# Performance work log

Hardware: AMD Instinct MI355X
Metric: run time of the kernel (lower is better)

The kernel has to match this reference:

```python
import jax, jax.numpy as jnp
import numpy as np

T, H, F, E, K = 4096, 2048, 1408, 8, 2  # tokens, hidden, intermediate, experts, top_k


def setup_inputs() -> dict:
    key = jax.random.key(0)
    k1, k2, k3, k4 = jax.random.split(key, 4)
    return {
        "hidden_states": jax.random.normal(k1, (T, H), dtype=jnp.float32),
        "router_logits": jax.random.normal(k2, (T, E), dtype=jnp.float32),
        # w1: (E, 2, H, F) where dim 1 = [gate_proj, up_proj]
        "w1": jax.random.normal(k3, (E, 2, H, F), dtype=jnp.float32) * 0.02,
        # w2: (E, F, H) down projection
        "w2": jax.random.normal(k4, (E, F, H), dtype=jnp.float32) * 0.02,
        "top_k": K,
    }


def reference(hidden_states, router_logits, w1, w2, top_k):
    # Router: softmax over all experts, then select top_k.
    # renormalize_topk_logits=False -> combine weights are the raw softmax probs.
    probs = jax.nn.softmax(router_logits, axis=-1)            # (T, E)
    topk_w, topk_ids = jax.lax.top_k(probs, top_k)            # (T, K) each

    num_experts = w1.shape[0]
    out = jnp.zeros_like(hidden_states)                       # (T, H)
    # Fixed small loop over experts (structurally distinct weight slices);
    # each expert's FFN is a dense GEMM over all tokens, masked by the
    # per-token combine coefficient (0 for tokens not routed to this expert).
    for e in range(num_experts):
        coef = jnp.sum(jnp.where(topk_ids == e, topk_w, 0.0), axis=-1)  # (T,)
        gate = hidden_states @ w1[e, 0]                       # (T, F)
        up = hidden_states @ w1[e, 1]                         # (T, F)
        h = jax.nn.silu(gate) * up                            # SwiGLU
        out = out + coef[:, None] * (h @ w2[e])               # (T, H)
    return out
```

## Files before the change

### kernel.cpp

```cpp
#include <hip/hip_runtime.h>
#include <stdint.h>

#define T_TOK 4096
#define HID   2048
#define FF    1408
#define NE    8
#define BUF   16384
#define NT1   (HID / 32)
#define NT2   (FF / 32)

typedef __attribute__((ext_vector_type(8))) short short8;
typedef __attribute__((ext_vector_type(4))) float f32x4;

__device__ inline unsigned short f2bf(float f) {
  uint32_t u = __builtin_bit_cast(uint32_t, f);
  u += 0x7fffu + ((u >> 16) & 1u);
  return (unsigned short)(u >> 16);
}

__device__ inline uint32_t cvt_pk(float a, float b) {
  uint32_t r;
  asm("v_cvt_pk_bf16_f32 %0, %1, %2" : "=v"(r) : "v"(a), "v"(b));
  return r;
}

__device__ inline void gload16(const void* g, void* l) {
  __builtin_amdgcn_global_load_lds(
      (const __attribute__((address_space(1))) unsigned int*)g,
      (__attribute__((address_space(3))) unsigned int*)l, 16, 0, 0);
}

__device__ inline void wait4_barrier() {
  asm volatile("s_waitcnt vmcnt(4)" ::: "memory");
  __builtin_amdgcn_s_barrier();
  asm volatile("" ::: "memory");
}
__device__ inline void wait0_barrier() {
  asm volatile("s_waitcnt vmcnt(0)" ::: "memory");
  __builtin_amdgcn_s_barrier();
  asm volatile("" ::: "memory");
}

__global__ __launch_bounds__(256) void route_kernel(const float* __restrict__ logits,
                                                    int2* __restrict__ eids,
                                                    float2* __restrict__ ecfs) {
  int t = blockIdx.x * 256 + threadIdx.x;
  const float4* lp = (const float4*)(logits + (size_t)t * NE);
  float4 a = lp[0], b = lp[1];
  float l[8] = {a.x, a.y, a.z, a.w, b.x, b.y, b.z, b.w};
  float mx = l[0];
#pragma unroll
  for (int i = 1; i < 8; ++i) mx = fmaxf(mx, l[i]);
  float s = 0.f, p[8];
#pragma unroll
  for (int i = 0; i < 8; ++i) { p[i] = __expf(l[i] - mx); s += p[i]; }
  float inv = 1.f / s;
  int e0 = 0;
#pragma unroll
  for (int i = 1; i < 8; ++i) if (l[i] > l[e0]) e0 = i;
  int e1 = (e0 == 0) ? 1 : 0;
#pragma unroll
  for (int i = 0; i < 8; ++i) if (i != e0 && l[i] > l[e1]) e1 = i;
  eids[t] = make_int2(e0, e1);
  ecfs[t] = make_float2(p[e0] * inv, p[e1] * inv);
}

__global__ __launch_bounds__(256) void compact_kernel(const int2* __restrict__ eids,
                                                      const float2* __restrict__ ecfs,
                                                      int* __restrict__ tok,
                                                      float* __restrict__ coef,
                                                      int* __restrict__ rowptr) {
  int e = blockIdx.x, tid = threadIdx.x;
  __shared__ int hist[8];
  __shared__ int wsum[4];
  __shared__ int runv;
  if (tid < 8) hist[tid] = 0;
  __syncthreads();
  for (int t = tid; t < T_TOK; t += 256) {
    int2 ei = eids[t];
    atomicAdd(&hist[ei.x], 1);
    atomicAdd(&hist[ei.y], 1);
  }
  __syncthreads();
  int off = 0;
  for (int j = 0; j < e; ++j) off += hist[j];
  if (tid == 0) {
    runv = 0;
    if (e == 0) rowptr[0] = 0;
    rowptr[e + 1] = off + hist[e];
  }
  __syncthreads();
  int wave = tid >> 6, lane = tid & 63;
  for (int c = 0; c < T_TOK; c += 256) {
    int t = c + tid;
    int2 ei = eids[t];
    float2 cf = ecfs[t];
    bool fl = false; float cv = 0.f;
    if (ei.x == e)      { fl = true; cv = cf.x; }
    else if (ei.y == e) { fl = true; cv = cf.y; }
    unsigned long long m = __ballot(fl);
    if (lane == 0) wsum[wave] = __popcll(m);
    __syncthreads();
    int woff = runv;
    for (int wv = 0; wv < wave; ++wv) woff += wsum[wv];
    int pos = off + woff + __popcll(m & ((1ull << lane) - 1ull));
    if (fl) { tok[pos] = t; coef[pos] = cv; }
    __syncthreads();
    if (tid == 0) runv += wsum[0] + wsum[1] + wsum[2] + wsum[3];
    __syncthreads();
  }
}

__global__ __launch_bounds__(256) void cvtx_kernel(const float* __restrict__ x,
                                                   unsigned short* __restrict__ xb) {
  int i = blockIdx.x * 256 + threadIdx.x;
  float4 v = ((const float4*)x)[i];
  uint2 o;
  o.x = cvt_pk(v.x, v.y);
  o.y = cvt_pk(v.z, v.w);
  ((uint2*)xb)[i] = o;
}

__global__ __launch_bounds__(256) void wcvt_kernel(const float* __restrict__ in,
                                                   unsigned short* __restrict__ out,
                                                   int R, int C) {
  __shared__ unsigned short t[64][72];
  const float* ip = in + ((size_t)blockIdx.z * R + blockIdx.y * 64) * C + blockIdx.x * 64;
  int tid = threadIdx.x;
  int r = tid >> 2, cg = (tid & 3) * 16;
  const float* rp = ip + (size_t)r * C + cg;
#pragma unroll
  for (int j = 0; j < 4; ++j) {
    float4 v = *(const float4*)(rp + j * 4);
    int c = cg + j * 4;
    t[c + 0][r] = f2bf(v.x);
    t[c + 1][r] = f2bf(v.y);
    t[c + 2][r] = f2bf(v.z);
    t[c + 3][r] = f2bf(v.w);
  }
  __syncthreads();
  int cr = tid >> 2, kg = (tid & 3) * 16;
  unsigned short* op = out + ((size_t)blockIdx.z * C + blockIdx.x * 64 + cr) * R +
                       blockIdx.y * 64 + kg;
  *(short8*)op = *(const short8*)&t[cr][kg];
  *(short8*)(op + 8) = *(const short8*)&t[cr][kg + 8];
}

__global__ __launch_bounds__(256) void gemm1_kernel(const unsigned short* __restrict__ Xb,
                                                    const unsigned short* __restrict__ w1t,
                                                    const int* __restrict__ tok,
                                                    const int* __restrict__ rowptr,
                                                    unsigned short* __restrict__ hbuf) {
  int f = blockIdx.x + 22 * blockIdx.y;
  int g = (f & 7) * 88 + (f >> 3);
  int ftile = g >> 5, mtile = g & 31;
  int e = blockIdx.z;
  int base = rowptr[e], cnt = rowptr[e + 1] - base;
  if (mtile * 128 >= cnt) return;
  __shared__ char smem[3 * BUF];
  int tid = threadIdx.x, lane = tid & 63, wave = tid >> 6;

  int rA = wave * 32 + (lane >> 2);
  int cd = (lane & 3) ^ ((rA >> 1) & 3);
  int sA0 = min(mtile * 128 + rA, cnt - 1);
  int sA1 = min(mtile * 128 + rA + 16, cnt - 1);
  const unsigned short* gA0 = Xb + (size_t)tok[base + sA0] * HID + cd * 8;
  const unsigned short* gA1 = Xb + (size_t)tok[base + sA1] * HID + cd * 8;
  int r1 = rA + 16;
  int p0 = (rA >> 4) & 1, f0 = (rA & 15) + 16 * (rA >> 5);
  int p1 = (r1 >> 4) & 1, f1 = (r1 & 15) + 16 * (r1 >> 5);
  const unsigned short* gB0 = w1t + ((size_t)(e * 2 + p0) * FF + ftile * 64 + f0) * HID + cd * 8;
  const unsigned short* gB1 = w1t + ((size_t)(e * 2 + p1) * FF + ftile * 64 + f1) * HID + cd * 8;
  int lb = wave * 2048 + lane * 16;

#define STG1(bp, k0) do {                          \
    gload16(gA0 + (k0), (bp) + lb);                \
    gload16(gA1 + (k0), (bp) + lb + 1024);         \
    gload16(gB0 + (k0), (bp) + 8192 + lb);         \
    gload16(gB1 + (k0), (bp) + 8192 + lb + 1024);  \
  } while (0)

  int wm = wave >> 1, wn = wave & 1, kc = lane >> 4;
  int aoff[4], boff[4];
#pragma unroll
  for (int mi = 0; mi < 4; ++mi) {
    int row = wm * 64 + mi * 16 + (lane & 15);
    aoff[mi] = row * 64 + ((kc ^ ((row >> 1) & 3)) << 4);
  }
#pragma unroll
  for (int ni = 0; ni < 4; ++ni) {
    int n = wn * 64 + ni * 16 + (lane & 15);
    boff[ni] = 8192 + n * 64 + ((kc ^ ((n >> 1) & 3)) << 4);
  }

  const f32x4 vz = {0.f, 0.f, 0.f, 0.f};
  f32x4 acc[4][4];
#pragma unroll
  for (int mi = 0; mi < 4; ++mi)
#pragma unroll
    for (int ni = 0; ni < 4; ++ni) acc[mi][ni] = vz;

  STG1(smem, 0);
  STG1(smem + BUF, 32);
  wait4_barrier();

  char* cur = smem;
  char* nxt = smem + 2 * BUF;
  for (int t = 0; t < NT1; ++t) {
    bool pf = (t + 2) < NT1;
    if (pf) STG1(nxt, (t + 2) * 32);
    short8 af[4], bb[4];
#pragma unroll
    for (int mi = 0; mi < 4; ++mi) af[mi] = *(const short8*)(cur + aoff[mi]);
#pragma unroll
    for (int ni = 0; ni < 4; ++ni) bb[ni] = *(const short8*)(cur + boff[ni]);
    __builtin_amdgcn_s_setprio(1);
#pragma unroll
    for (int mi = 0; mi < 4; ++mi)
#pragma unroll
      for (int ni = 0; ni < 4; ++ni)
        acc[mi][ni] = __builtin_amdgcn_mfma_f32_16x16x32_bf16(af[mi], bb[ni], acc[mi][ni], 0, 0, 0);
    __builtin_amdgcn_s_setprio(0);
    if (pf) wait4_barrier(); else wait0_barrier();
    cur = (cur == smem + 2 * BUF) ? smem : cur + BUF;
    nxt = (nxt == smem + 2 * BUF) ? smem : nxt + BUF;
  }
#undef STG1

  int fb = ftile * 64 + wn * 32 + (lane & 15);
#pragma unroll
  for (int mi = 0; mi < 4; ++mi) {
#pragma unroll
    for (int i = 0; i < 4; ++i) {
      int ml = wm * 64 + mi * 16 + (lane >> 4) * 4 + i;
      int slot = mtile * 128 + ml;
      if (slot < cnt) {
        size_t hrow = (size_t)(base + slot) * FF + fb;
        float g0 = acc[mi][0][i], u0 = acc[mi][1][i];
        float g1 = acc[mi][2][i], u1 = acc[mi][3][i];
        hbuf[hrow]      = f2bf(g0 / (1.f + __expf(-g0)) * u0);
        hbuf[hrow + 16] = f2bf(g1 / (1.f + __expf(-g1)) * u1);
      }
    }
  }
}

__global__ __launch_bounds__(256) void gemm2_kernel(const unsigned short* __restrict__ hbuf,
                                                    const unsigned short* __restrict__ w2t,
                                                    const int* __restrict__ tok,
                                                    const float* __restrict__ coef,
                                                    const int* __restrict__ rowptr,
                                                    float* __restrict__ out) {
  int f = blockIdx.x + 16 * blockIdx.y;
  int g = (f & 7) * 64 + (f >> 3);
  int ntile = g >> 5, mtile = g & 31;
  int e = blockIdx.z;
  int base = rowptr[e], cnt = rowptr[e + 1] - base;
  if (mtile * 128 >= cnt) return;
  __shared__ char smem[3 * BUF];
  __shared__ int tokL[128];
  __shared__ float cofL[128];
  int tid = threadIdx.x, lane = tid & 63, wave = tid >> 6;
  if (tid < 128) {
    int slot = min(mtile * 128 + tid, cnt - 1);
    tokL[tid] = tok[base + slot];
    cofL[tid] = coef[base + slot];
  }
  __syncthreads();

  int rA = wave * 32 + (lane >> 2);
  int cd = (lane & 3) ^ ((rA >> 1) & 3);
  int sA0 = min(mtile * 128 + rA, cnt - 1);
  int sA1 = min(mtile * 128 + rA + 16, cnt - 1);
  const unsigned short* gA0 = hbuf + (size_t)(base + sA0) * FF + cd * 8;
  const unsigned short* gA1 = hbuf + (size_t)(base + sA1) * FF + cd * 8;
  const unsigned short* gB0 = w2t + ((size_t)e * HID + ntile * 128 + rA) * FF + cd * 8;
  const unsigned short* gB1 = gB0 + (size_t)16 * FF;
  int lb = wave * 2048 + lane * 16;

#define STG2(bp, k0) do {                          \
    gload16(gA0 + (k0), (bp) + lb);                \
    gload16(gA1 + (k0), (bp) + lb + 1024);         \
    gload16(gB0 + (k0), (bp) + 8192 + lb);         \
    gload16(gB1 + (k0), (bp) + 8192 + lb + 1024);  \
  } while (0)

  int wm = wave >> 1, wn = wave & 1, kc = lane >> 4;
  int aoff[4], boff[4];
#pragma unroll
  for (int mi = 0; mi < 4; ++mi) {
    int row = wm * 64 + mi * 16 + (lane & 15);
    aoff[mi] = row * 64 + ((kc ^ ((row >> 1) & 3)) << 4);
  }
#pragma unroll
  for (int ni = 0; ni < 4; ++ni) {
    int n = wn * 64 + ni * 16 + (lane & 15);
    boff[ni] = 8192 + n * 64 + ((kc ^ ((n >> 1) & 3)) << 4);
  }

  const f32x4 vz = {0.f, 0.f, 0.f, 0.f};
  f32x4 acc[4][4];
#pragma unroll
  for (int mi = 0; mi < 4; ++mi)
#pragma unroll
    for (int ni = 0; ni < 4; ++ni) acc[mi][ni] = vz;

  STG2(smem, 0);
  STG2(smem + BUF, 32);
  wait4_barrier();

  char* cur = smem;
  char* nxt = smem + 2 * BUF;
  for (int t = 0; t < NT2; ++t) {
    bool pf = (t + 2) < NT2;
    if (pf) STG2(nxt, (t + 2) * 32);
    short8 af[4], bb[4];
#pragma unroll
    for (int mi = 0; mi < 4; ++mi) af[mi] = *(const short8*)(cur + aoff[mi]);
#pragma unroll
    for (int ni = 0; ni < 4; ++ni) bb[ni] = *(const short8*)(cur + boff[ni]);
    __builtin_amdgcn_s_setprio(1);
#pragma unroll
    for (int mi = 0; mi < 4; ++mi)
#pragma unroll
      for (int ni = 0; ni < 4; ++ni)
        acc[mi][ni] = __builtin_amdgcn_mfma_f32_16x16x32_bf16(af[mi], bb[ni], acc[mi][ni], 0, 0, 0);
    __builtin_amdgcn_s_setprio(0);
    if (pf) wait4_barrier(); else wait0_barrier();
    cur = (cur == smem + 2 * BUF) ? smem : cur + BUF;
    nxt = (nxt == smem + 2 * BUF) ? smem : nxt + BUF;
  }
#undef STG2

#pragma unroll
  for (int mi = 0; mi < 4; ++mi) {
#pragma unroll
    for (int i = 0; i < 4; ++i) {
      int ml = wm * 64 + mi * 16 + (lane >> 4) * 4 + i;
      int slot = mtile * 128 + ml;
      if (slot < cnt) {
        float cf = cofL[ml];
        float* op = out + (size_t)tokL[ml] * HID + ntile * 128 + wn * 64 + (lane & 15);
#pragma unroll
        for (int ni = 0; ni < 4; ++ni)
          unsafeAtomicAdd(op + ni * 16, cf * acc[mi][ni][i]);
      }
    }
  }
}

extern "C" void kernel_launch(void* const* d_in, const int* in_sizes, int n_in,
                              void* d_out, int out_size, void* d_ws, size_t ws_size,
                              hipStream_t stream) {
  const float* X  = (const float*)d_in[0];
  const float* RL = (const float*)d_in[1];
  const float* W1 = (const float*)d_in[2];
  const float* W2 = (const float*)d_in[3];
  float* out = (float*)d_out;

  const size_t OFF_EIDS = 4096;
  const size_t OFF_ECFS = 36864;
  const size_t OFF_TOK  = 69632;
  const size_t OFF_COEF = 102400;
  const size_t OFF_XB   = 135168;
  const size_t OFF_H    = 16912384;
  const size_t OFF_W1T  = 39981056;
  const size_t OFF_W2T  = 132255744;
  const size_t TOTAL2   = 178393088;
  if (ws_size < TOTAL2 || n_in < 4) return;

  char* w = (char*)d_ws;
  int*    rowptr = (int*)w;
  int2*   eids   = (int2*)(w + OFF_EIDS);
  float2* ecfs   = (float2*)(w + OFF_ECFS);
  int*    tok    = (int*)(w + OFF_TOK);
  float*  coef   = (float*)(w + OFF_COEF);
  unsigned short* Xb   = (unsigned short*)(w + OFF_XB);
  unsigned short* hbuf = (unsigned short*)(w + OFF_H);
  unsigned short* w1t  = (unsigned short*)(w + OFF_W1T);
  unsigned short* w2t  = (unsigned short*)(w + OFF_W2T);

  hipMemsetAsync(d_out, 0, (size_t)T_TOK * HID * sizeof(float), stream);
  route_kernel<<<T_TOK / 256, 256, 0, stream>>>(RL, eids, ecfs);
  compact_kernel<<<NE, 256, 0, stream>>>(eids, ecfs, tok, coef, rowptr);
  cvtx_kernel<<<(T_TOK * HID / 4) / 256, 256, 0, stream>>>(X, Xb);
  wcvt_kernel<<<dim3(FF / 64, HID / 64, NE * 2), 256, 0, stream>>>(W1, w1t, HID, FF);
  wcvt_kernel<<<dim3(HID / 64, FF / 64, NE), 256, 0, stream>>>(W2, w2t, FF, HID);
  gemm1_kernel<<<dim3(FF / 64, T_TOK / 128, NE), 256, 0, stream>>>(Xb, w1t, tok, rowptr, hbuf);
  gemm2_kernel<<<dim3(HID / 128, T_TOK / 128, NE), 256, 0, stream>>>(hbuf, w2t, tok, coef, rowptr, out);
}
```

Before: 368.6 us.

## Replace atomic scatter in down-proj with dense store plus combine; deepen gemm1 pipeline

The down-projection GEMM now writes unweighted per-slot rows to a dense buffer that reuses the W1 bf16 workspace. A new combine kernel then gathers each token's two expert rows via an inverse map and applies the routing weights. This drops the output memset and the fp32 atomic adds, at the cost of an extra 2x T x H fp32 buffer pass. Gemm1 also moves from 3-stage to 4-stage LDS buffering with three tiles in flight. The new path runs only if the workspace is large enough, otherwise the old atomic path is used.

```diff
diff --git a/kernel.cpp b/kernel.cpp
--- a/kernel.cpp
+++ b/kernel.cpp
@@ -30,6 +30,11 @@
       (__attribute__((address_space(3))) unsigned int*)l, 16, 0, 0);
 }
 
+__device__ inline void wait8_barrier() {
+  asm volatile("s_waitcnt vmcnt(8)" ::: "memory");
+  __builtin_amdgcn_s_barrier();
+  asm volatile("" ::: "memory");
+}
 __device__ inline void wait4_barrier() {
   asm volatile("s_waitcnt vmcnt(4)" ::: "memory");
   __builtin_amdgcn_s_barrier();
@@ -69,7 +74,8 @@
                                                       const float2* __restrict__ ecfs,
                                                       int* __restrict__ tok,
                                                       float* __restrict__ coef,
-                                                      int* __restrict__ rowptr) {
+                                                      int* __restrict__ rowptr,
+                                                      int* __restrict__ invm) {
   int e = blockIdx.x, tid = threadIdx.x;
   __shared__ int hist[8];
   __shared__ int wsum[4];
@@ -95,16 +101,16 @@
     int t = c + tid;
     int2 ei = eids[t];
     float2 cf = ecfs[t];
-    bool fl = false; float cv = 0.f;
-    if (ei.x == e)      { fl = true; cv = cf.x; }
-    else if (ei.y == e) { fl = true; cv = cf.y; }
+    bool fl = false; float cv = 0.f; int ks = 0;
+    if (ei.x == e)      { fl = true; cv = cf.x; ks = 0; }
+    else if (ei.y == e) { fl = true; cv = cf.y; ks = 1; }
     unsigned long long m = __ballot(fl);
     if (lane == 0) wsum[wave] = __popcll(m);
     __syncthreads();
     int woff = runv;
     for (int wv = 0; wv < wave; ++wv) woff += wsum[wv];
     int pos = off + woff + __popcll(m & ((1ull << lane) - 1ull));
-    if (fl) { tok[pos] = t; coef[pos] = cv; }
+    if (fl) { tok[pos] = t; coef[pos] = cv; invm[2 * t + ks] = pos; }
     __syncthreads();
     if (tid == 0) runv += wsum[0] + wsum[1] + wsum[2] + wsum[3];
     __syncthreads();
@@ -157,7 +163,7 @@
   int e = blockIdx.z;
   int base = rowptr[e], cnt = rowptr[e + 1] - base;
   if (mtile * 128 >= cnt) return;
-  __shared__ char smem[3 * BUF];
+  __shared__ char smem[4 * BUF];
   int tid = threadIdx.x, lane = tid & 63, wave = tid >> 6;
 
   int rA = wave * 32 + (lane >> 2);
@@ -202,13 +208,13 @@
 
   STG1(smem, 0);
   STG1(smem + BUF, 32);
-  wait4_barrier();
-
-  char* cur = smem;
-  char* nxt = smem + 2 * BUF;
+  STG1(smem + 2 * BUF, 64);
+  wait8_barrier();
+
   for (int t = 0; t < NT1; ++t) {
-    bool pf = (t + 2) < NT1;
-    if (pf) STG1(nxt, (t + 2) * 32);
+    char* cur = smem + (t & 3) * BUF;
+    bool pf = (t + 3) < NT1;
+    if (pf) STG1(smem + ((t + 3) & 3) * BUF, (t + 3) * 32);
     short8 af[4], bb[4];
 #pragma unroll
     for (int mi = 0; mi < 4; ++mi) af[mi] = *(const short8*)(cur + aoff[mi]);
@@ -221,9 +227,9 @@
       for (int ni = 0; ni < 4; ++ni)
         acc[mi][ni] = __builtin_amdgcn_mfma_f32_16x16x32_bf16(af[mi], bb[ni], acc[mi][ni], 0, 0, 0);
     __builtin_amdgcn_s_setprio(0);
-    if (pf) wait4_barrier(); else wait0_barrier();
-    cur = (cur == smem + 2 * BUF) ? smem : cur + BUF;
-    nxt = (nxt == smem + 2 * BUF) ? smem : nxt + BUF;
+    if (pf) wait8_barrier();
+    else if (t + 2 < NT1) wait4_barrier();
+    else wait0_barrier();
   }
 #undef STG1
 
@@ -246,6 +252,117 @@
 }
 
 __global__ __launch_bounds__(256) void gemm2_kernel(const unsigned short* __restrict__ hbuf,
+                                                    const unsigned short* __restrict__ w2t,
+                                                    const int* __restrict__ rowptr,
+                                                    float* __restrict__ obuf) {
+  int f = blockIdx.x + 16 * blockIdx.y;
+  int g = (f & 7) * 64 + (f >> 3);
+  int ntile = g >> 5, mtile = g & 31;
+  int e = blockIdx.z;
+  int base = rowptr[e], cnt = rowptr[e + 1] - base;
+  if (mtile * 128 >= cnt) return;
+  __shared__ char smem[3 * BUF];
+  int tid = threadIdx.x, lane = tid & 63, wave = tid >> 6;
+
+  int rA = wave * 32 + (lane >> 2);
+  int cd = (lane & 3) ^ ((rA >> 1) & 3);
+  int sA0 = min(mtile * 128 + rA, cnt - 1);
+  int sA1 = min(mtile * 128 + rA + 16, cnt - 1);
+  const unsigned short* gA0 = hbuf + (size_t)(base + sA0) * FF + cd * 8;
+  const unsigned short* gA1 = hbuf + (size_t)(base + sA1) * FF + cd * 8;
+  const unsigned short* gB0 = w2t + ((size_t)e * HID + ntile * 128 + rA) * FF + cd * 8;
+  const unsigned short* gB1 = gB0 + (size_t)16 * FF;
+  int lb = wave * 2048 + lane * 16;
+
+#define STG2(bp, k0) do {                          \
+    gload16(gA0 + (k0), (bp) + lb);                \
+    gload16(gA1 + (k0), (bp) + lb + 1024);         \
+    gload16(gB0 + (k0), (bp) + 8192 + lb);         \
+    gload16(gB1 + (k0), (bp) + 8192 + lb + 1024);  \
+  } while (0)
+
+  int wm = wave >> 1, wn = wave & 1, kc = lane >> 4;
+  int aoff[4], boff[4];
+#pragma unroll
+  for (int mi = 0; mi < 4; ++mi) {
+    int row = wm * 64 + mi * 16 + (lane & 15);
+    aoff[mi] = row * 64 + ((kc ^ ((row >> 1) & 3)) << 4);
+  }
+#pragma unroll
+  for (int ni = 0; ni < 4; ++ni) {
+    int n = wn * 64 + ni * 16 + (lane & 15);
+    boff[ni] = 8192 + n * 64 + ((kc ^ ((n >> 1) & 3)) << 4);
+  }
+
+  const f32x4 vz = {0.f, 0.f, 0.f, 0.f};
+  f32x4 acc[4][4];
+#pragma unroll
+  for (int mi = 0; mi < 4; ++mi)
+#pragma unroll
+    for (int ni = 0; ni < 4; ++ni) acc[mi][ni] = vz;
+
+  STG2(smem, 0);
+  STG2(smem + BUF, 32);
+  wait4_barrier();
+
+  char* cur = smem;
+  char* nxt = smem + 2 * BUF;
+  for (int t = 0; t < NT2; ++t) {
+    bool pf = (t + 2) < NT2;
+    if (pf) STG2(nxt, (t + 2) * 32);
+    short8 af[4], bb[4];
+#pragma unroll
+    for (int mi = 0; mi < 4; ++mi) af[mi] = *(const short8*)(cur + aoff[mi]);
+#pragma unroll
+    for (int ni = 0; ni < 4; ++ni) bb[ni] = *(const short8*)(cur + boff[ni]);
+    __builtin_amdgcn_s_setprio(1);
+#pragma unroll
+    for (int mi = 0; mi < 4; ++mi)
+#pragma unroll
+      for (int ni = 0; ni < 4; ++ni)
+        acc[mi][ni] = __builtin_amdgcn_mfma_f32_16x16x32_bf16(af[mi], bb[ni], acc[mi][ni], 0, 0, 0);
+    __builtin_amdgcn_s_setprio(0);
+    if (pf) wait4_barrier(); else wait0_barrier();
+    cur = (cur == smem + 2 * BUF) ? smem : cur + BUF;
+    nxt = (nxt == smem + 2 * BUF) ? smem : nxt + BUF;
+  }
+#undef STG2
+
+  int nb = ntile * 128 + wn * 64 + (lane & 15);
+#pragma unroll
+  for (int mi = 0; mi < 4; ++mi) {
+#pragma unroll
+    for (int i = 0; i < 4; ++i) {
+      int ml = wm * 64 + mi * 16 + (lane >> 4) * 4 + i;
+      int slot = mtile * 128 + ml;
+      if (slot < cnt) {
+        float* op = obuf + (size_t)(base + slot) * HID + nb;
+#pragma unroll
+        for (int ni = 0; ni < 4; ++ni) op[ni * 16] = acc[mi][ni][i];
+      }
+    }
+  }
+}
+
+__global__ __launch_bounds__(256) void combine_kernel(const float* __restrict__ obuf,
+                                                      const int2* __restrict__ invm,
+                                                      const float* __restrict__ coef,
+                                                      float* __restrict__ out) {
+  int idx = blockIdx.x * 256 + threadIdx.x;
+  int t = idx >> 9, h4 = idx & 511;
+  int2 pp = invm[t];
+  float c0 = coef[pp.x], c1 = coef[pp.y];
+  float4 a = ((const float4*)(obuf + (size_t)pp.x * HID))[h4];
+  float4 b = ((const float4*)(obuf + (size_t)pp.y * HID))[h4];
+  float4 o;
+  o.x = c0 * a.x + c1 * b.x;
+  o.y = c0 * a.y + c1 * b.y;
+  o.z = c0 * a.z + c1 * b.z;
+  o.w = c0 * a.w + c1 * b.w;
+  ((float4*)out)[idx] = o;
+}
+
+__global__ __launch_bounds__(256) void gemm2_atomic(const unsigned short* __restrict__ hbuf,
                                                     const unsigned short* __restrict__ w2t,
                                                     const int* __restrict__ tok,
                                                     const float* __restrict__ coef,
@@ -278,7 +395,7 @@
   const unsigned short* gB1 = gB0 + (size_t)16 * FF;
   int lb = wave * 2048 + lane * 16;
 
-#define STG2(bp, k0) do {                          \
+#define STG2F(bp, k0) do {                         \
     gload16(gA0 + (k0), (bp) + lb);                \
     gload16(gA1 + (k0), (bp) + lb + 1024);         \
     gload16(gB0 + (k0), (bp) + 8192 + lb);         \
@@ -305,15 +422,15 @@
 #pragma unroll
     for (int ni = 0; ni < 4; ++ni) acc[mi][ni] = vz;
 
-  STG2(smem, 0);
-  STG2(smem + BUF, 32);
+  STG2F(smem, 0);
+  STG2F(smem + BUF, 32);
   wait4_barrier();
 
   char* cur = smem;
   char* nxt = smem + 2 * BUF;
   for (int t = 0; t < NT2; ++t) {
     bool pf = (t + 2) < NT2;
-    if (pf) STG2(nxt, (t + 2) * 32);
+    if (pf) STG2F(nxt, (t + 2) * 32);
     short8 af[4], bb[4];
 #pragma unroll
     for (int mi = 0; mi < 4; ++mi) af[mi] = *(const short8*)(cur + aoff[mi]);
@@ -330,7 +447,7 @@
     cur = (cur == smem + 2 * BUF) ? smem : cur + BUF;
     nxt = (nxt == smem + 2 * BUF) ? smem : nxt + BUF;
   }
-#undef STG2
+#undef STG2F
 
 #pragma unroll
   for (int mi = 0; mi < 4; ++mi) {
@@ -367,7 +484,10 @@
   const size_t OFF_W1T  = 39981056;
   const size_t OFF_W2T  = 132255744;
   const size_t TOTAL2   = 178393088;
+  const size_t OFF_INV  = 178393088;
+  const size_t TOTAL3   = 178425856;
   if (ws_size < TOTAL2 || n_in < 4) return;
+  bool big = ws_size >= TOTAL3;
 
   char* w = (char*)d_ws;
   int*    rowptr = (int*)w;
@@ -379,13 +499,20 @@
   unsigned short* hbuf = (unsigned short*)(w + OFF_H);
   unsigned short* w1t  = (unsigned short*)(w + OFF_W1T);
   unsigned short* w2t  = (unsigned short*)(w + OFF_W2T);
-
-  hipMemsetAsync(d_out, 0, (size_t)T_TOK * HID * sizeof(float), stream);
+  float* obuf = (float*)(w + OFF_W1T);
+  int* invm = big ? (int*)(w + OFF_INV) : (int*)hbuf;
+
+  if (!big) hipMemsetAsync(d_out, 0, (size_t)T_TOK * HID * sizeof(float), stream);
   route_kernel<<<T_TOK / 256, 256, 0, stream>>>(RL, eids, ecfs);
-  compact_kernel<<<NE, 256, 0, stream>>>(eids, ecfs, tok, coef, rowptr);
+  compact_kernel<<<NE, 256, 0, stream>>>(eids, ecfs, tok, coef, rowptr, invm);
   cvtx_kernel<<<(T_TOK * HID / 4) / 256, 256, 0, stream>>>(X, Xb);
   wcvt_kernel<<<dim3(FF / 64, HID / 64, NE * 2), 256, 0, stream>>>(W1, w1t, HID, FF);
   wcvt_kernel<<<dim3(HID / 64, FF / 64, NE), 256, 0, stream>>>(W2, w2t, FF, HID);
   gemm1_kernel<<<dim3(FF / 64, T_TOK / 128, NE), 256, 0, stream>>>(Xb, w1t, tok, rowptr, hbuf);
-  gemm2_kernel<<<dim3(HID / 128, T_TOK / 128, NE), 256, 0, stream>>>(hbuf, w2t, tok, coef, rowptr, out);
-}
+  if (big) {
+    gemm2_kernel<<<dim3(HID / 128, T_TOK / 128, NE), 256, 0, stream>>>(hbuf, w2t, rowptr, obuf);
+    combine_kernel<<<(T_TOK * HID / 4) / 256, 256, 0, stream>>>(obuf, (const int2*)invm, coef, out);
+  } else {
+    gemm2_atomic<<<dim3(HID / 128, T_TOK / 128, NE), 256, 0, stream>>>(hbuf, w2t, tok, coef, rowptr, out);
+  }
+}
```

After: 345.6 us, median of 3. 1.07x faster.
